# Kernel optimization log

Measured on AMD Instinct MI355X. Metric: run time of the kernel, lower is better.

The kernel has to match this reference:

```python
import jax, jax.numpy as jnp
import numpy as np

H, N, M, F, D = 8, 4096, 4096, 1024, 256

def setup_inputs() -> dict:
    key = jax.random.key(0)
    ks = jax.random.split(key, 8)
    sc = 0.02
    return {
        "this": jax.random.normal(ks[0], (N, F), dtype=jnp.float32),
        "that": jax.random.normal(ks[1], (M, F), dtype=jnp.float32),
        "mask": jax.random.randint(ks[2], (N, M), 0, 2) > 0,
        "Wq": jax.random.normal(ks[3], (H, F, D), dtype=jnp.float32) * sc,
        "bq": jnp.zeros((H, D), dtype=jnp.float32),
        "Wk": jax.random.normal(ks[4], (H, F, D), dtype=jnp.float32) * sc,
        "bk": jnp.zeros((H, D), dtype=jnp.float32),
        "Wv": jax.random.normal(ks[5], (H, F, D), dtype=jnp.float32) * sc,
        "bv": jnp.zeros((H, D), dtype=jnp.float32),
        "Wo": jax.random.normal(ks[6], (2 * F, F), dtype=jnp.float32) * sc,
        "bo": jnp.zeros((F,), dtype=jnp.float32),
    }

def reference(this, that, mask, Wq, bq, Wk, bk, Wv, bv, Wo, bo):
    # Per-head projections, batched over heads. q:[h,n,d] k,v:[h,m,d]
    q = jnp.einsum('nf,hfd->hnd', this, Wq) + bq[:, None, :]
    k = jnp.einsum('mf,hfd->hmd', that, Wk) + bk[:, None, :]
    v = jnp.einsum('mf,hfd->hmd', that, Wv) + bv[:, None, :]
    # Unscaled attention scores [h,n,m]
    s = jnp.einsum('hnd,hmd->hnm', q, k)
    neg = 1e9 * (~mask).astype(s.dtype)              # additive mask [n,m]
    head_ids = jnp.arange(s.shape[0])[:, None, None]  # mask applies to heads >= 4 only
    s = jnp.where(head_ids >= 4, s - neg, s)
    w = jax.nn.softmax(s, axis=-1)
    r = jnp.einsum('hnm,hmd->hnd', w, v)              # [h,n,d]
    # concat heads along feature axis in head order -> [n, h*d]
    cat = jnp.transpose(r, (1, 0, 2)).reshape(this.shape[0], -1)
    out = cat @ Wo + bo
    return out + this
```

## Files before the change

### kernel.cpp

```cpp
#include <hip/hip_runtime.h>
#include <stdint.h>


#define H_ 8
#define N_ 4096
#define M_ 4096
#define F_ 1024
#define D_ 256

typedef unsigned short u16;
typedef unsigned int u32;
typedef unsigned long long u64;
typedef __bf16 bf16x8 __attribute__((ext_vector_type(8)));
typedef float f32x4 __attribute__((ext_vector_type(4)));

static __device__ __forceinline__ u16 f2bf(float f) {
  union { float f; u32 u; } v; v.f = f;
  u32 u = v.u + 0x7fffu + ((v.u >> 16) & 1u);
  return (u16)(u >> 16);
}

static __device__ __forceinline__ void gld16(const void* g, void* l) {
  __builtin_amdgcn_global_load_lds(
      (const __attribute__((address_space(1))) void*)g,
      (__attribute__((address_space(3))) void*)l, 16, 0, 0);
}

__global__ void k_mask_detect(const u32* __restrict__ m, u32* __restrict__ flag) {
  u32 bad = 0;
  for (int i = threadIdx.x; i < 4096; i += 64) bad |= (m[i] & ~1u);
  u64 anyBad = __ballot(bad != 0);
  if (threadIdx.x == 0) *flag = (anyBad != 0) ? 1u : 0u;
}

__global__ void k_mask_pack(const void* __restrict__ mp, const u32* __restrict__ flag,
                            u64* __restrict__ out) {
  const int i = blockIdx.x * 256 + threadIdx.x;
  u64 bits = 0;
  if (*flag) {
    const u32* p = (const u32*)mp + (size_t)i * 16;
#pragma unroll
    for (int w = 0; w < 16; ++w) {
      u32 x = p[w];
#pragma unroll
      for (int j = 0; j < 4; ++j)
        bits |= (u64)(((x >> (8 * j)) & 0xffu) ? 1u : 0u) << (w * 4 + j);
    }
  } else {
    const u32* p = (const u32*)mp + (size_t)i * 64;
#pragma unroll
    for (int w = 0; w < 64; ++w) bits |= (u64)(p[w] ? 1u : 0u) << w;
  }
  out[i] = bits;
}

__global__ void k_f32_to_bf16(const float* __restrict__ in, u16* __restrict__ out, int n4) {
  int i = blockIdx.x * blockDim.x + threadIdx.x;
  if (i >= n4) return;
  float4 v = ((const float4*)in)[i];
  u32 w0 = (u32)f2bf(v.x) | ((u32)f2bf(v.y) << 16);
  u32 w1 = (u32)f2bf(v.z) | ((u32)f2bf(v.w) << 16);
  ((uint2*)out)[i] = make_uint2(w0, w1);
}

__global__ void k_transpose_f32_bf16(const float* __restrict__ in, u16* __restrict__ out,
                                     int R, int C) {
  __shared__ float t[32][33];
  const int b = blockIdx.z;
  const float* src = in + (size_t)b * R * C;
  u16* dst = out + (size_t)b * R * C;
  const int r0 = blockIdx.x * 32, c0 = blockIdx.y * 32;
  const int tr = threadIdx.x >> 3, tc = (threadIdx.x & 7) * 4;
  float4 v = *(const float4*)(src + (size_t)(r0 + tr) * C + c0 + tc);
  t[tr][tc + 0] = v.x; t[tr][tc + 1] = v.y; t[tr][tc + 2] = v.z; t[tr][tc + 3] = v.w;
  __syncthreads();
  u16* d4 = dst + (size_t)(c0 + tr) * R + r0 + tc;
  d4[0] = f2bf(t[tc + 0][tr]); d4[1] = f2bf(t[tc + 1][tr]);
  d4[2] = f2bf(t[tc + 2][tr]); d4[3] = f2bf(t[tc + 3][tr]);
}

__global__ void k_transpose_bf16(const u16* __restrict__ in, u16* __restrict__ out,
                                 int R, int C) {
  __shared__ u16 t[32][33];
  const int b = blockIdx.z;
  const u16* src = in + (size_t)b * R * C;
  u16* dst = out + (size_t)b * R * C;
  const int r0 = blockIdx.x * 32, c0 = blockIdx.y * 32;
  const int tr = threadIdx.x >> 3, tc = (threadIdx.x & 7) * 4;
  const u16* s4 = src + (size_t)(r0 + tr) * C + c0 + tc;
  t[tr][tc + 0] = s4[0]; t[tr][tc + 1] = s4[1]; t[tr][tc + 2] = s4[2]; t[tr][tc + 3] = s4[3];
  __syncthreads();
  u16* d4 = dst + (size_t)(c0 + tr) * R + r0 + tc;
  d4[0] = t[tc + 0][tr]; d4[1] = t[tc + 1][tr]; d4[2] = t[tc + 2][tr]; d4[3] = t[tc + 3][tr];
}

template <int EPI>
__global__ __launch_bounds__(256, 2) void k_gemm_nt(
    const u16* __restrict__ A, const u16* __restrict__ B,
    const float* __restrict__ bias, const float* __restrict__ resid,
    u16* __restrict__ Cb, float* __restrict__ Cf,
    int K, int lda, int ldb, int ldc,
    size_t aBatch, size_t bBatch, size_t biasBatch, size_t cBatch)
{
  __shared__ u16 la[128 * 64];
  __shared__ u16 lb[128 * 64];
  const int tid = threadIdx.x;
  const int lane = tid & 63, wave = tid >> 6;
  const int g = lane >> 4, fr = lane & 15;
  const int wr = wave >> 1, wc = wave & 1;
  const int z = blockIdx.z;
  const size_t row0 = (size_t)blockIdx.x * 128, col0 = (size_t)blockIdx.y * 128;
  const u16* Ab = A + z * aBatch + row0 * lda;
  const u16* Bb = B + z * bBatch + col0 * ldb;

  f32x4 zero = {0.f, 0.f, 0.f, 0.f};
  f32x4 acc[4][4];
#pragma unroll
  for (int m = 0; m < 4; ++m)
#pragma unroll
    for (int n = 0; n < 4; ++n) acc[m][n] = zero;

  for (int k0 = 0; k0 < K; k0 += 64) {
    __syncthreads();
#pragma unroll
    for (int i = 0; i < 4; ++i) {
      int c = i * 256 + tid;
      int row = c >> 3, slot = c & 7;
      int srcSlot = slot ^ (row & 7);
      gld16(Ab + (size_t)row * lda + k0 + srcSlot * 8, la + (size_t)(i * 256 + wave * 64) * 8);
      gld16(Bb + (size_t)row * ldb + k0 + srcSlot * 8, lb + (size_t)(i * 256 + wave * 64) * 8);
    }
    __syncthreads();
#pragma unroll
    for (int kk = 0; kk < 2; ++kk) {
      const int colByte = (kk * 32 + g * 8) * 2;
      bf16x8 af[4], bfr[4];
#pragma unroll
      for (int m = 0; m < 4; ++m) {
        int row = wr * 64 + m * 16 + fr;
        af[m] = *(const bf16x8*)((const char*)la + ((row * 128 + colByte) ^ ((row & 7) << 4)));
      }
#pragma unroll
      for (int n = 0; n < 4; ++n) {
        int row = wc * 64 + n * 16 + fr;
        bfr[n] = *(const bf16x8*)((const char*)lb + ((row * 128 + colByte) ^ ((row & 7) << 4)));
      }
#pragma unroll
      for (int m = 0; m < 4; ++m)
#pragma unroll
        for (int n = 0; n < 4; ++n)
          acc[m][n] = __builtin_amdgcn_mfma_f32_16x16x32_bf16(af[m], bfr[n], acc[m][n], 0, 0, 0);
    }
  }

#pragma unroll
  for (int n = 0; n < 4; ++n) {
    const int col = wc * 64 + n * 16 + fr;
    const float bv = bias[z * biasBatch + col0 + col];
#pragma unroll
    for (int m = 0; m < 4; ++m) {
#pragma unroll
      for (int r = 0; r < 4; ++r) {
        const int row = wr * 64 + m * 16 + g * 4 + r;
        const float val = acc[m][n][r] + bv;
        const size_t idx = z * cBatch + (row0 + row) * ldc + col0 + col;
        if (EPI == 0) {
          Cb[idx] = f2bf(val);
        } else {
          Cf[idx] = val + resid[(row0 + row) * ldc + col0 + col];
        }
      }
    }
  }
}

__global__ __launch_bounds__(256, 2) void k_attn(
    const u16* __restrict__ q, const u16* __restrict__ k,
    const u16* __restrict__ vt, const u64* __restrict__ mbits,
    u16* __restrict__ cat)
{
  __shared__ u16 smem[32768];
  u16* lk = smem;
  u16* lv = smem + 16384;
  const int tid = threadIdx.x;
  const int lane = tid & 63, wave = tid >> 6;
  const int g = lane >> 4, fr = lane & 15;
  const int h = blockIdx.y;
  const int n0 = blockIdx.x * 64 + wave * 16;
  const u16* qh = q + ((size_t)h * N_ + n0 + fr) * D_;
  const u16* kh = k + (size_t)h * M_ * D_;
  const u16* vh = vt + (size_t)h * D_ * M_;

  bf16x8 qf[8];
#pragma unroll
  for (int dc = 0; dc < 8; ++dc) qf[dc] = *(const bf16x8*)(qh + dc * 32 + g * 8);

  f32x4 zero = {0.f, 0.f, 0.f, 0.f};
  f32x4 racc[16];
#pragma unroll
  for (int i = 0; i < 16; ++i) racc[i] = zero;
  float mrow = -3e38f, lrow = 0.f;

  const u64* mrp = mbits + (size_t)(n0 + fr) * (M_ / 64);
  const bool useMask = (h >= 4);

  for (int m0 = 0; m0 < M_; m0 += 64) {
    __syncthreads();
#pragma unroll
    for (int i = 0; i < 8; ++i) {
      int c = i * 256 + tid;
      int row = c >> 5, slot = c & 31;
      int srcSlot = (slot & 24) | ((slot ^ row) & 7);
      gld16(kh + (size_t)(m0 + row) * D_ + srcSlot * 8, lk + (size_t)(i * 256 + wave * 64) * 8);
      int row2 = c >> 3, slot2 = c & 7;
      int srcSlot2 = (slot2 ^ row2) & 7;
      gld16(vh + (size_t)row2 * M_ + m0 + srcSlot2 * 8, lv + (size_t)(i * 256 + wave * 64) * 8);
    }
    __syncthreads();

    f32x4 s[4];
#pragma unroll
    for (int mt = 0; mt < 4; ++mt) s[mt] = zero;
#pragma unroll
    for (int dc = 0; dc < 8; ++dc) {
      const int colByte = (dc * 32 + g * 8) * 2;
#pragma unroll
      for (int mt = 0; mt < 4; ++mt) {
        const int row = mt * 16 + fr;
        bf16x8 af = *(const bf16x8*)((const char*)lk + ((row * 512 + colByte) ^ ((row & 7) << 4)));
        s[mt] = __builtin_amdgcn_mfma_f32_16x16x32_bf16(af, qf[dc], s[mt], 0, 0, 0);
      }
    }

    if (useMask) {
      const u64 wm = mrp[m0 >> 6];
#pragma unroll
      for (int mt = 0; mt < 4; ++mt) {
        const u32 nib = (u32)(wm >> (mt * 16 + g * 4));
        if (!(nib & 1u)) s[mt][0] -= 1e9f;
        if (!(nib & 2u)) s[mt][1] -= 1e9f;
        if (!(nib & 4u)) s[mt][2] -= 1e9f;
        if (!(nib & 8u)) s[mt][3] -= 1e9f;
      }
    }

    float pm = -3e38f;
#pragma unroll
    for (int mt = 0; mt < 4; ++mt)
#pragma unroll
      for (int r = 0; r < 4; ++r) pm = fmaxf(pm, s[mt][r]);
    pm = fmaxf(pm, __shfl_xor(pm, 16, 64));
    pm = fmaxf(pm, __shfl_xor(pm, 32, 64));
    const float mnew = fmaxf(mrow, pm);
    const float scale = __expf(mrow - mnew);
    float ls = 0.f;
#pragma unroll
    for (int mt = 0; mt < 4; ++mt)
#pragma unroll
      for (int r = 0; r < 4; ++r) { float p = __expf(s[mt][r] - mnew); s[mt][r] = p; ls += p; }
    ls += __shfl_xor(ls, 16, 64);
    ls += __shfl_xor(ls, 32, 64);
    lrow = lrow * scale + ls;
    mrow = mnew;
#pragma unroll
    for (int i = 0; i < 16; ++i) racc[i] *= scale;

    u32 w[4][2];
#pragma unroll
    for (int mt = 0; mt < 4; ++mt) {
      w[mt][0] = (u32)f2bf(s[mt][0]) | ((u32)f2bf(s[mt][1]) << 16);
      w[mt][1] = (u32)f2bf(s[mt][2]) | ((u32)f2bf(s[mt][3]) << 16);
    }
    const int src0 = (g & 1) * 32 + fr;
    const int src1 = src0 + 16;
    const bool hi = (g >> 1) != 0;
#pragma unroll
    for (int cc = 0; cc < 2; ++cc) {
      u32 a0 = __shfl(w[cc * 2][0], src0, 64), b0 = __shfl(w[cc * 2 + 1][0], src0, 64);
      u32 a1 = __shfl(w[cc * 2][1], src0, 64), b1 = __shfl(w[cc * 2 + 1][1], src0, 64);
      u32 a2 = __shfl(w[cc * 2][0], src1, 64), b2 = __shfl(w[cc * 2 + 1][0], src1, 64);
      u32 a3 = __shfl(w[cc * 2][1], src1, 64), b3 = __shfl(w[cc * 2 + 1][1], src1, 64);
      union { u32 u[4]; bf16x8 v; } pf;
      pf.u[0] = hi ? b0 : a0;
      pf.u[1] = hi ? b1 : a1;
      pf.u[2] = hi ? b2 : a2;
      pf.u[3] = hi ? b3 : a3;
      const int mcolByte = (cc * 32 + g * 8) * 2;
#pragma unroll
      for (int dt = 0; dt < 16; ++dt) {
        const int row = dt * 16 + fr;
        bf16x8 av = *(const bf16x8*)((const char*)lv + ((row * 128 + mcolByte) ^ ((row & 7) << 4)));
        racc[dt] = __builtin_amdgcn_mfma_f32_16x16x32_bf16(av, pf.v, racc[dt], 0, 0, 0);
      }
    }
  }

  __syncthreads();
  u16* lt = smem + (size_t)wave * (16 * 264);
  const float inv = 1.f / lrow;
#pragma unroll
  for (int dt = 0; dt < 16; ++dt) {
    u32 w0 = (u32)f2bf(racc[dt][0] * inv) | ((u32)f2bf(racc[dt][1] * inv) << 16);
    u32 w1 = (u32)f2bf(racc[dt][2] * inv) | ((u32)f2bf(racc[dt][3] * inv) << 16);
    *(u32*)(lt + fr * 264 + dt * 16 + g * 4) = w0;
    *(u32*)(lt + fr * 264 + dt * 16 + g * 4 + 2) = w1;
  }
  __syncthreads();
#pragma unroll
  for (int p = 0; p < 8; ++p) {
    const int c2 = p * 64 + lane;
    const int row = c2 >> 5, ch = c2 & 31;
    uint4 val = *(const uint4*)(lt + row * 264 + ch * 8);
    *(uint4*)(cat + (size_t)(n0 + row) * (H_ * D_) + (size_t)h * D_ + ch * 8) = val;
  }
}

extern "C" void kernel_launch(void* const* d_in, const int* in_sizes, int n_in,
                              void* d_out, int out_size, void* d_ws, size_t ws_size,
                              hipStream_t stream) {
  const float* thisf = (const float*)d_in[0];
  const float* thatf = (const float*)d_in[1];
  const void* maskp = (const void*)d_in[2];
  const float* Wq = (const float*)d_in[3];
  const float* bq = (const float*)d_in[4];
  const float* Wk = (const float*)d_in[5];
  const float* bk = (const float*)d_in[6];
  const float* Wv = (const float*)d_in[7];
  const float* bv = (const float*)d_in[8];
  const float* Wo = (const float*)d_in[9];
  const float* bo = (const float*)d_in[10];
  float* outp = (float*)d_out;

  char* ws = (char*)d_ws;
  size_t o = 0;
  u16* thisb = (u16*)(ws + o); o += (size_t)N_ * F_ * 2;
  u16* thatb = (u16*)(ws + o); o += (size_t)M_ * F_ * 2;
  u16* wqt = (u16*)(ws + o); o += (size_t)H_ * D_ * F_ * 2;
  u16* wkt = (u16*)(ws + o); o += (size_t)H_ * D_ * F_ * 2;
  u16* wvt = (u16*)(ws + o); o += (size_t)H_ * D_ * F_ * 2;
  u16* wot = (u16*)(ws + o); o += (size_t)F_ * 2 * F_ * 2;
  u16* qb = (u16*)(ws + o); o += (size_t)H_ * N_ * D_ * 2;
  u16* kb = (u16*)(ws + o); o += (size_t)H_ * M_ * D_ * 2;
  u16* vb = (u16*)(ws + o); o += (size_t)H_ * M_ * D_ * 2;
  u16* vtb = (u16*)(ws + o); o += (size_t)H_ * D_ * M_ * 2;
  u16* catb = (u16*)(ws + o); o += (size_t)N_ * 2 * F_ * 2;
  u64* mbits = (u64*)(ws + o); o += (size_t)N_ * M_ / 8;
  u32* mflag = (u32*)(ws + o); o += 256;
  (void)ws_size; (void)in_sizes; (void)n_in; (void)out_size;

  k_mask_detect<<<dim3(1), dim3(64), 0, stream>>>((const u32*)maskp, mflag);
  k_mask_pack<<<dim3(N_ * M_ / 64 / 256), dim3(256), 0, stream>>>(maskp, mflag, mbits);

  k_f32_to_bf16<<<dim3(N_ * F_ / 4 / 256), dim3(256), 0, stream>>>(thisf, thisb, N_ * F_ / 4);
  k_f32_to_bf16<<<dim3(M_ * F_ / 4 / 256), dim3(256), 0, stream>>>(thatf, thatb, M_ * F_ / 4);
  k_transpose_f32_bf16<<<dim3(F_ / 32, D_ / 32, H_), dim3(256), 0, stream>>>(Wq, wqt, F_, D_);
  k_transpose_f32_bf16<<<dim3(F_ / 32, D_ / 32, H_), dim3(256), 0, stream>>>(Wk, wkt, F_, D_);
  k_transpose_f32_bf16<<<dim3(F_ / 32, D_ / 32, H_), dim3(256), 0, stream>>>(Wv, wvt, F_, D_);
  k_transpose_f32_bf16<<<dim3(2 * F_ / 32, F_ / 32, 1), dim3(256), 0, stream>>>(Wo, wot, 2 * F_, F_);

  k_gemm_nt<0><<<dim3(N_ / 128, D_ / 128, H_), dim3(256), 0, stream>>>(
      thisb, wqt, bq, nullptr, qb, nullptr, F_, F_, F_, D_,
      (size_t)0, (size_t)D_ * F_, (size_t)D_, (size_t)N_ * D_);
  k_gemm_nt<0><<<dim3(M_ / 128, D_ / 128, H_), dim3(256), 0, stream>>>(
      thatb, wkt, bk, nullptr, kb, nullptr, F_, F_, F_, D_,
      (size_t)0, (size_t)D_ * F_, (size_t)D_, (size_t)M_ * D_);
  k_gemm_nt<0><<<dim3(M_ / 128, D_ / 128, H_), dim3(256), 0, stream>>>(
      thatb, wvt, bv, nullptr, vb, nullptr, F_, F_, F_, D_,
      (size_t)0, (size_t)D_ * F_, (size_t)D_, (size_t)M_ * D_);

  k_transpose_bf16<<<dim3(M_ / 32, D_ / 32, H_), dim3(256), 0, stream>>>(vb, vtb, M_, D_);

  k_attn<<<dim3(N_ / 64, H_), dim3(256), 0, stream>>>(qb, kb, vtb, mbits, catb);

  k_gemm_nt<1><<<dim3(N_ / 128, F_ / 128, 1), dim3(256), 0, stream>>>(
      catb, wot, bo, thisf, nullptr, outp, 2 * F_, 2 * F_, 2 * F_, F_,
      (size_t)0, (size_t)0, (size_t)0, (size_t)0);
}
```

Before: 551.3 us.

## Rewrite attention with 32x32 MFMA, pre-swizzled K/V layouts, and double-buffered GEMM

The attention kernel is rewritten to use 32x32x16 bf16 MFMA tiles with 32 query rows per wave, a double-buffered K/V LDS pipeline, exp2-based softmax and a lazy rescale that only runs when the row max grows past a threshold. The K and V projection GEMMs now write directly into blocked layouts the attention kernel can stream, which removes the separate V transpose kernel. The mask is packed with a wave ballot into a column-major word layout. The generic GEMM gains LDS double buffering. The lazy-rescale threshold and the new layouts add numerical and indexing risk in exchange for higher MFMA throughput and fewer passes over memory.

```diff
diff --git a/kernel.cpp b/kernel.cpp
--- a/kernel.cpp
+++ b/kernel.cpp
@@ -11,13 +11,21 @@
 typedef unsigned short u16;
 typedef unsigned int u32;
 typedef unsigned long long u64;
+typedef unsigned char u8;
 typedef __bf16 bf16x8 __attribute__((ext_vector_type(8)));
 typedef float f32x4 __attribute__((ext_vector_type(4)));
+typedef float f32x16 __attribute__((ext_vector_type(16)));
 
 static __device__ __forceinline__ u16 f2bf(float f) {
   union { float f; u32 u; } v; v.f = f;
   u32 u = v.u + 0x7fffu + ((v.u >> 16) & 1u);
   return (u16)(u >> 16);
+}
+
+static __device__ __forceinline__ u32 cvtpk(float lo, float hi) {
+  u32 r;
+  asm("v_cvt_pk_bf16_f32 %0, %1, %2" : "=v"(r) : "v"(lo), "v"(hi));
+  return r;
 }
 
 static __device__ __forceinline__ void gld16(const void* g, void* l) {
@@ -33,25 +41,20 @@
   if (threadIdx.x == 0) *flag = (anyBad != 0) ? 1u : 0u;
 }
 
-__global__ void k_mask_pack(const void* __restrict__ mp, const u32* __restrict__ flag,
-                            u64* __restrict__ out) {
-  const int i = blockIdx.x * 256 + threadIdx.x;
-  u64 bits = 0;
-  if (*flag) {
-    const u32* p = (const u32*)mp + (size_t)i * 16;
-#pragma unroll
-    for (int w = 0; w < 16; ++w) {
-      u32 x = p[w];
-#pragma unroll
-      for (int j = 0; j < 4; ++j)
-        bits |= (u64)(((x >> (8 * j)) & 0xffu) ? 1u : 0u) << (w * 4 + j);
-    }
-  } else {
-    const u32* p = (const u32*)mp + (size_t)i * 64;
-#pragma unroll
-    for (int w = 0; w < 64; ++w) bits |= (u64)(p[w] ? 1u : 0u) << w;
-  }
-  out[i] = bits;
+__global__ void k_mask_pack2(const void* __restrict__ mp, const u32* __restrict__ flag,
+                             u32* __restrict__ out) {
+  const int lane = threadIdx.x & 63, wave = threadIdx.x >> 6;
+  const int wid = blockIdx.x * 4 + wave;
+  const int qrow = wid >> 6;
+  const int m0 = (wid & 63) * 64;
+  int x;
+  if (*flag) x = ((const u8*)mp)[(size_t)qrow * M_ + m0 + lane];
+  else       x = ((const int*)mp)[(size_t)qrow * M_ + m0 + lane];
+  u64 bits = __ballot(x != 0);
+  if (lane == 0) {
+    out[(size_t)(m0 >> 5) * N_ + qrow] = (u32)bits;
+    out[(size_t)((m0 >> 5) + 1) * N_ + qrow] = (u32)(bits >> 32);
+  }
 }
 
 __global__ void k_f32_to_bf16(const float* __restrict__ in, u16* __restrict__ out, int n4) {
@@ -79,21 +82,6 @@
   d4[2] = f2bf(t[tc + 2][tr]); d4[3] = f2bf(t[tc + 3][tr]);
 }
 
-__global__ void k_transpose_bf16(const u16* __restrict__ in, u16* __restrict__ out,
-                                 int R, int C) {
-  __shared__ u16 t[32][33];
-  const int b = blockIdx.z;
-  const u16* src = in + (size_t)b * R * C;
-  u16* dst = out + (size_t)b * R * C;
-  const int r0 = blockIdx.x * 32, c0 = blockIdx.y * 32;
-  const int tr = threadIdx.x >> 3, tc = (threadIdx.x & 7) * 4;
-  const u16* s4 = src + (size_t)(r0 + tr) * C + c0 + tc;
-  t[tr][tc + 0] = s4[0]; t[tr][tc + 1] = s4[1]; t[tr][tc + 2] = s4[2]; t[tr][tc + 3] = s4[3];
-  __syncthreads();
-  u16* d4 = dst + (size_t)(c0 + tr) * R + r0 + tc;
-  d4[0] = t[tc + 0][tr]; d4[1] = t[tc + 1][tr]; d4[2] = t[tc + 2][tr]; d4[3] = t[tc + 3][tr];
-}
-
 template <int EPI>
 __global__ __launch_bounds__(256, 2) void k_gemm_nt(
     const u16* __restrict__ A, const u16* __restrict__ B,
@@ -102,8 +90,8 @@
     int K, int lda, int ldb, int ldc,
     size_t aBatch, size_t bBatch, size_t biasBatch, size_t cBatch)
 {
-  __shared__ u16 la[128 * 64];
-  __shared__ u16 lb[128 * 64];
+  __shared__ u16 la[2][128 * 64];
+  __shared__ u16 lb[2][128 * 64];
   const int tid = threadIdx.x;
   const int lane = tid & 63, wave = tid >> 6;
   const int g = lane >> 4, fr = lane & 15;
@@ -120,17 +108,24 @@
 #pragma unroll
     for (int n = 0; n < 4; ++n) acc[m][n] = zero;
 
-  for (int k0 = 0; k0 < K; k0 += 64) {
-    __syncthreads();
+  auto STAGE = [&](int bs, int k0) {
 #pragma unroll
     for (int i = 0; i < 4; ++i) {
       int c = i * 256 + tid;
       int row = c >> 3, slot = c & 7;
       int srcSlot = slot ^ (row & 7);
-      gld16(Ab + (size_t)row * lda + k0 + srcSlot * 8, la + (size_t)(i * 256 + wave * 64) * 8);
-      gld16(Bb + (size_t)row * ldb + k0 + srcSlot * 8, lb + (size_t)(i * 256 + wave * 64) * 8);
-    }
-    __syncthreads();
+      gld16(Ab + (size_t)row * lda + k0 + srcSlot * 8, &la[bs][(i * 256 + wave * 64) * 8]);
+      gld16(Bb + (size_t)row * ldb + k0 + srcSlot * 8, &lb[bs][(i * 256 + wave * 64) * 8]);
+    }
+  };
+
+  STAGE(0, 0);
+  __syncthreads();
+  int cur = 0;
+  for (int k0 = 0; k0 < K; k0 += 64) {
+    if (k0 + 64 < K) STAGE(cur ^ 1, k0 + 64);
+    const char* lac = (const char*)la[cur];
+    const char* lbc = (const char*)lb[cur];
 #pragma unroll
     for (int kk = 0; kk < 2; ++kk) {
       const int colByte = (kk * 32 + g * 8) * 2;
@@ -138,12 +133,12 @@
 #pragma unroll
       for (int m = 0; m < 4; ++m) {
         int row = wr * 64 + m * 16 + fr;
-        af[m] = *(const bf16x8*)((const char*)la + ((row * 128 + colByte) ^ ((row & 7) << 4)));
+        af[m] = *(const bf16x8*)(lac + ((row * 128 + colByte) ^ ((row & 7) << 4)));
       }
 #pragma unroll
       for (int n = 0; n < 4; ++n) {
         int row = wc * 64 + n * 16 + fr;
-        bfr[n] = *(const bf16x8*)((const char*)lb + ((row * 128 + colByte) ^ ((row & 7) << 4)));
+        bfr[n] = *(const bf16x8*)(lbc + ((row * 128 + colByte) ^ ((row & 7) << 4)));
       }
 #pragma unroll
       for (int m = 0; m < 4; ++m)
@@ -151,6 +146,8 @@
         for (int n = 0; n < 4; ++n)
           acc[m][n] = __builtin_amdgcn_mfma_f32_16x16x32_bf16(af[m], bfr[n], acc[m][n], 0, 0, 0);
     }
+    __syncthreads();
+    cur ^= 1;
   }
 
 #pragma unroll
@@ -163,155 +160,168 @@
       for (int r = 0; r < 4; ++r) {
         const int row = wr * 64 + m * 16 + g * 4 + r;
         const float val = acc[m][n][r] + bv;
-        const size_t idx = z * cBatch + (row0 + row) * ldc + col0 + col;
+        const size_t grow = row0 + row, gcol = col0 + col;
         if (EPI == 0) {
-          Cb[idx] = f2bf(val);
+          Cb[(size_t)z * cBatch + grow * ldc + gcol] = f2bf(val);
+        } else if (EPI == 1) {
+          Cb[(size_t)z * (M_ * D_) + (gcol >> 3) * (M_ * 8) + grow * 8 + (gcol & 7)] = f2bf(val);
+        } else if (EPI == 2) {
+          Cb[(size_t)z * (M_ * D_) + (grow >> 3) * (D_ * 8) + gcol * 8 + (grow & 7)] = f2bf(val);
         } else {
-          Cf[idx] = val + resid[(row0 + row) * ldc + col0 + col];
+          Cf[grow * ldc + gcol] = val + resid[grow * ldc + gcol];
         }
       }
     }
   }
 }
 
-__global__ __launch_bounds__(256, 2) void k_attn(
-    const u16* __restrict__ q, const u16* __restrict__ k,
-    const u16* __restrict__ vt, const u64* __restrict__ mbits,
+__global__ __launch_bounds__(256, 2) void k_attn2(
+    const u16* __restrict__ q, const u16* __restrict__ k2,
+    const u16* __restrict__ v2, const u32* __restrict__ mw,
     u16* __restrict__ cat)
 {
   __shared__ u16 smem[32768];
-  u16* lk = smem;
-  u16* lv = smem + 16384;
   const int tid = threadIdx.x;
   const int lane = tid & 63, wave = tid >> 6;
-  const int g = lane >> 4, fr = lane & 15;
-  const int h = blockIdx.y;
-  const int n0 = blockIdx.x * 64 + wave * 16;
-  const u16* qh = q + ((size_t)h * N_ + n0 + fr) * D_;
-  const u16* kh = k + (size_t)h * M_ * D_;
-  const u16* vh = vt + (size_t)h * D_ * M_;
-
-  bf16x8 qf[8];
-#pragma unroll
-  for (int dc = 0; dc < 8; ++dc) qf[dc] = *(const bf16x8*)(qh + dc * 32 + g * 8);
-
-  f32x4 zero = {0.f, 0.f, 0.f, 0.f};
-  f32x4 racc[16];
-#pragma unroll
-  for (int i = 0; i < 16; ++i) racc[i] = zero;
+  const int hi = lane >> 5, col = lane & 31;
+  const int h = blockIdx.x & 7;
+  const int xt = blockIdx.x >> 3;
+  const int n0w = xt * 128 + wave * 32;
+  const float L2E = 1.44269504f;
+
+  const u16* kh = k2 + (size_t)h * (M_ * D_);
+  const u16* vh = v2 + (size_t)h * (M_ * D_);
+
+  bf16x8 qf[16];
+  {
+    const u16* qp = q + ((size_t)h * N_ + n0w + col) * D_ + hi * 8;
+#pragma unroll
+    for (int dc = 0; dc < 16; ++dc) qf[dc] = *(const bf16x8*)(qp + dc * 16);
+  }
+
+  f32x16 racc[8];
+#pragma unroll
+  for (int i = 0; i < 8; ++i)
+#pragma unroll
+    for (int e = 0; e < 16; ++e) racc[i][e] = 0.f;
+
   float mrow = -3e38f, lrow = 0.f;
-
-  const u64* mrp = mbits + (size_t)(n0 + fr) * (M_ / 64);
   const bool useMask = (h >= 4);
-
-  for (int m0 = 0; m0 < M_; m0 += 64) {
+  const u32* mp = mw + (n0w + col);
+
+  auto STAGE = [&](int bs, int m0) {
+    u16* lkb = smem + bs * 16384;
+    u16* lvb = lkb + 8192;
+#pragma unroll
+    for (int i = 0; i < 4; ++i) {
+      int c = i * 256 + tid;
+      gld16(kh + (size_t)(c >> 5) * (M_ * 8) + (size_t)(m0 + (c & 31)) * 8,
+            lkb + (i * 256 + wave * 64) * 8);
+      gld16(vh + (size_t)(c >> 8) * (D_ * 8) + (size_t)m0 * 256 + (size_t)(c & 255) * 8,
+            lvb + (i * 256 + wave * 64) * 8);
+    }
+  };
+
+  STAGE(0, 0);
+  __syncthreads();
+  int cur = 0;
+
+  for (int it = 0; it < M_ / 32; ++it) {
+    const int m0 = it * 32;
+    if (it + 1 < M_ / 32) STAGE(cur ^ 1, m0 + 32);
+    u32 mword = 0xFFFFFFFFu;
+    if (useMask) mword = mp[(size_t)(m0 >> 5) * N_];
+
+    const char* lkb = (const char*)smem + cur * 32768;
+    const char* lvb = lkb + 16384;
+
+    f32x16 sA, sB;
+#pragma unroll
+    for (int e = 0; e < 16; ++e) { sA[e] = 0.f; sB[e] = 0.f; }
+#pragma unroll
+    for (int dc = 0; dc < 16; dc += 2) {
+      bf16x8 a0 = *(const bf16x8*)(lkb + dc * 1024 + lane * 16);
+      bf16x8 a1 = *(const bf16x8*)(lkb + dc * 1024 + 1024 + lane * 16);
+      sA = __builtin_amdgcn_mfma_f32_32x32x16_bf16(a0, qf[dc], sA, 0, 0, 0);
+      sB = __builtin_amdgcn_mfma_f32_32x32x16_bf16(a1, qf[dc + 1], sB, 0, 0, 0);
+    }
+    f32x16 sv = sA + sB;
+
+    if (useMask) {
+      u32 mm = mword >> (hi * 4);
+#pragma unroll
+      for (int r = 0; r < 16; ++r)
+        if (!((mm >> ((r & 3) + 8 * (r >> 2))) & 1u)) sv[r] -= 1e9f;
+    }
+
+    float pm = sv[0];
+#pragma unroll
+    for (int r = 1; r < 16; ++r) pm = fmaxf(pm, sv[r]);
+    pm = fmaxf(pm, __shfl_xor(pm, 32));
+
+    if (!__all(pm <= mrow + 8.f)) {
+      float mnew = fmaxf(mrow, pm);
+      float rs = __builtin_exp2f((mrow - mnew) * L2E);
+      lrow *= rs;
+#pragma unroll
+      for (int i = 0; i < 8; ++i)
+#pragma unroll
+        for (int e = 0; e < 16; ++e) racc[i][e] *= rs;
+      mrow = mnew;
+    }
+    const float mL = mrow * L2E;
+    float p[16];
+    float ls = 0.f;
+#pragma unroll
+    for (int r = 0; r < 16; ++r) {
+      p[r] = __builtin_exp2f(sv[r] * L2E - mL);
+      ls += p[r];
+    }
+    ls += __shfl_xor(ls, 32);
+    lrow += ls;
+
+#pragma unroll
+    for (int ks = 0; ks < 2; ++ks) {
+      u32 a0 = cvtpk(p[8 * ks + 0], p[8 * ks + 1]);
+      u32 a1 = cvtpk(p[8 * ks + 2], p[8 * ks + 3]);
+      u32 b0 = cvtpk(p[8 * ks + 4], p[8 * ks + 5]);
+      u32 b1 = cvtpk(p[8 * ks + 6], p[8 * ks + 7]);
+      u32 sa0 = __shfl_xor(a0, 32), sa1 = __shfl_xor(a1, 32);
+      u32 sb0 = __shfl_xor(b0, 32), sb1 = __shfl_xor(b1, 32);
+      union { u32 w[4]; bf16x8 v; } bp;
+      bp.w[0] = hi ? sb0 : a0;
+      bp.w[1] = hi ? sb1 : a1;
+      bp.w[2] = hi ? b0 : sa0;
+      bp.w[3] = hi ? b1 : sa1;
+      const char* lvk = lvb + ks * 8192 + hi * 4096 + col * 16;
+#pragma unroll
+      for (int ds = 0; ds < 8; ++ds) {
+        bf16x8 av = *(const bf16x8*)(lvk + ds * 512);
+        racc[ds] = __builtin_amdgcn_mfma_f32_32x32x16_bf16(av, bp.v, racc[ds], 0, 0, 0);
+      }
+    }
     __syncthreads();
-#pragma unroll
-    for (int i = 0; i < 8; ++i) {
-      int c = i * 256 + tid;
-      int row = c >> 5, slot = c & 31;
-      int srcSlot = (slot & 24) | ((slot ^ row) & 7);
-      gld16(kh + (size_t)(m0 + row) * D_ + srcSlot * 8, lk + (size_t)(i * 256 + wave * 64) * 8);
-      int row2 = c >> 3, slot2 = c & 7;
-      int srcSlot2 = (slot2 ^ row2) & 7;
-      gld16(vh + (size_t)row2 * M_ + m0 + srcSlot2 * 8, lv + (size_t)(i * 256 + wave * 64) * 8);
-    }
-    __syncthreads();
-
-    f32x4 s[4];
-#pragma unroll
-    for (int mt = 0; mt < 4; ++mt) s[mt] = zero;
-#pragma unroll
-    for (int dc = 0; dc < 8; ++dc) {
-      const int colByte = (dc * 32 + g * 8) * 2;
-#pragma unroll
-      for (int mt = 0; mt < 4; ++mt) {
-        const int row = mt * 16 + fr;
-        bf16x8 af = *(const bf16x8*)((const char*)lk + ((row * 512 + colByte) ^ ((row & 7) << 4)));
-        s[mt] = __builtin_amdgcn_mfma_f32_16x16x32_bf16(af, qf[dc], s[mt], 0, 0, 0);
-      }
-    }
-
-    if (useMask) {
-      const u64 wm = mrp[m0 >> 6];
-#pragma unroll
-      for (int mt = 0; mt < 4; ++mt) {
-        const u32 nib = (u32)(wm >> (mt * 16 + g * 4));
-        if (!(nib & 1u)) s[mt][0] -= 1e9f;
-        if (!(nib & 2u)) s[mt][1] -= 1e9f;
-        if (!(nib & 4u)) s[mt][2] -= 1e9f;
-        if (!(nib & 8u)) s[mt][3] -= 1e9f;
-      }
-    }
-
-    float pm = -3e38f;
-#pragma unroll
-    for (int mt = 0; mt < 4; ++mt)
-#pragma unroll
-      for (int r = 0; r < 4; ++r) pm = fmaxf(pm, s[mt][r]);
-    pm = fmaxf(pm, __shfl_xor(pm, 16, 64));
-    pm = fmaxf(pm, __shfl_xor(pm, 32, 64));
-    const float mnew = fmaxf(mrow, pm);
-    const float scale = __expf(mrow - mnew);
-    float ls = 0.f;
-#pragma unroll
-    for (int mt = 0; mt < 4; ++mt)
-#pragma unroll
-      for (int r = 0; r < 4; ++r) { float p = __expf(s[mt][r] - mnew); s[mt][r] = p; ls += p; }
-    ls += __shfl_xor(ls, 16, 64);
-    ls += __shfl_xor(ls, 32, 64);
-    lrow = lrow * scale + ls;
-    mrow = mnew;
-#pragma unroll
-    for (int i = 0; i < 16; ++i) racc[i] *= scale;
-
-    u32 w[4][2];
-#pragma unroll
-    for (int mt = 0; mt < 4; ++mt) {
-      w[mt][0] = (u32)f2bf(s[mt][0]) | ((u32)f2bf(s[mt][1]) << 16);
-      w[mt][1] = (u32)f2bf(s[mt][2]) | ((u32)f2bf(s[mt][3]) << 16);
-    }
-    const int src0 = (g & 1) * 32 + fr;
-    const int src1 = src0 + 16;
-    const bool hi = (g >> 1) != 0;
-#pragma unroll
-    for (int cc = 0; cc < 2; ++cc) {
-      u32 a0 = __shfl(w[cc * 2][0], src0, 64), b0 = __shfl(w[cc * 2 + 1][0], src0, 64);
-      u32 a1 = __shfl(w[cc * 2][1], src0, 64), b1 = __shfl(w[cc * 2 + 1][1], src0, 64);
-      u32 a2 = __shfl(w[cc * 2][0], src1, 64), b2 = __shfl(w[cc * 2 + 1][0], src1, 64);
-      u32 a3 = __shfl(w[cc * 2][1], src1, 64), b3 = __shfl(w[cc * 2 + 1][1], src1, 64);
-      union { u32 u[4]; bf16x8 v; } pf;
-      pf.u[0] = hi ? b0 : a0;
-      pf.u[1] = hi ? b1 : a1;
-      pf.u[2] = hi ? b2 : a2;
-      pf.u[3] = hi ? b3 : a3;
-      const int mcolByte = (cc * 32 + g * 8) * 2;
-#pragma unroll
-      for (int dt = 0; dt < 16; ++dt) {
-        const int row = dt * 16 + fr;
-        bf16x8 av = *(const bf16x8*)((const char*)lv + ((row * 128 + mcolByte) ^ ((row & 7) << 4)));
-        racc[dt] = __builtin_amdgcn_mfma_f32_16x16x32_bf16(av, pf.v, racc[dt], 0, 0, 0);
-      }
-    }
-  }
-
+    cur ^= 1;
+  }
+
+  char* lt = (char*)smem + wave * 16384;
+  const float inv = 1.f / lrow;
+#pragma unroll
+  for (int ds = 0; ds < 8; ++ds) {
+#pragma unroll
+    for (int t = 0; t < 8; ++t) {
+      int d0 = ds * 32 + (2 * t & 3) + 8 * (t >> 1) + 4 * hi;
+      u32 w = cvtpk(racc[ds][2 * t] * inv, racc[ds][2 * t + 1] * inv);
+      *(u32*)(lt + ((col * 512 + d0 * 2) ^ ((col & 7) << 4))) = w;
+    }
+  }
   __syncthreads();
-  u16* lt = smem + (size_t)wave * (16 * 264);
-  const float inv = 1.f / lrow;
-#pragma unroll
-  for (int dt = 0; dt < 16; ++dt) {
-    u32 w0 = (u32)f2bf(racc[dt][0] * inv) | ((u32)f2bf(racc[dt][1] * inv) << 16);
-    u32 w1 = (u32)f2bf(racc[dt][2] * inv) | ((u32)f2bf(racc[dt][3] * inv) << 16);
-    *(u32*)(lt + fr * 264 + dt * 16 + g * 4) = w0;
-    *(u32*)(lt + fr * 264 + dt * 16 + g * 4 + 2) = w1;
-  }
-  __syncthreads();
-#pragma unroll
-  for (int p = 0; p < 8; ++p) {
-    const int c2 = p * 64 + lane;
-    const int row = c2 >> 5, ch = c2 & 31;
-    uint4 val = *(const uint4*)(lt + row * 264 + ch * 8);
-    *(uint4*)(cat + (size_t)(n0 + row) * (H_ * D_) + (size_t)h * D_ + ch * 8) = val;
+#pragma unroll
+  for (int pch = 0; pch < 16; ++pch) {
+    int c = pch * 64 + lane;
+    int row = c >> 5, ch = c & 31;
+    uint4 val = *(const uint4*)(lt + ((row * 512 + ch * 16) ^ ((row & 7) << 4)));
+    *(uint4*)(cat + (size_t)(n0w + row) * (H_ * D_) + (size_t)h * D_ + ch * 8) = val;
   }
 }
 
@@ -339,17 +349,16 @@
   u16* wkt = (u16*)(ws + o); o += (size_t)H_ * D_ * F_ * 2;
   u16* wvt = (u16*)(ws + o); o += (size_t)H_ * D_ * F_ * 2;
   u16* wot = (u16*)(ws + o); o += (size_t)F_ * 2 * F_ * 2;
-  u16* qb = (u16*)(ws + o); o += (size_t)H_ * N_ * D_ * 2;
-  u16* kb = (u16*)(ws + o); o += (size_t)H_ * M_ * D_ * 2;
-  u16* vb = (u16*)(ws + o); o += (size_t)H_ * M_ * D_ * 2;
-  u16* vtb = (u16*)(ws + o); o += (size_t)H_ * D_ * M_ * 2;
+  u16* qb  = (u16*)(ws + o); o += (size_t)H_ * N_ * D_ * 2;
+  u16* k2  = (u16*)(ws + o); o += (size_t)H_ * M_ * D_ * 2;
+  u16* v2  = (u16*)(ws + o); o += (size_t)H_ * M_ * D_ * 2;
   u16* catb = (u16*)(ws + o); o += (size_t)N_ * 2 * F_ * 2;
-  u64* mbits = (u64*)(ws + o); o += (size_t)N_ * M_ / 8;
+  u32* mw2 = (u32*)(ws + o); o += (size_t)(M_ / 32) * N_ * 4;
   u32* mflag = (u32*)(ws + o); o += 256;
   (void)ws_size; (void)in_sizes; (void)n_in; (void)out_size;
 
   k_mask_detect<<<dim3(1), dim3(64), 0, stream>>>((const u32*)maskp, mflag);
-  k_mask_pack<<<dim3(N_ * M_ / 64 / 256), dim3(256), 0, stream>>>(maskp, mflag, mbits);
+  k_mask_pack2<<<dim3(N_ * (M_ / 64) / 4), dim3(256), 0, stream>>>(maskp, mflag, mw2);
 
   k_f32_to_bf16<<<dim3(N_ * F_ / 4 / 256), dim3(256), 0, stream>>>(thisf, thisb, N_ * F_ / 4);
   k_f32_to_bf16<<<dim3(M_ * F_ / 4 / 256), dim3(256), 0, stream>>>(thatf, thatb, M_ * F_ / 4);
@@ -361,18 +370,16 @@
   k_gemm_nt<0><<<dim3(N_ / 128, D_ / 128, H_), dim3(256), 0, stream>>>(
       thisb, wqt, bq, nullptr, qb, nullptr, F_, F_, F_, D_,
       (size_t)0, (size_t)D_ * F_, (size_t)D_, (size_t)N_ * D_);
-  k_gemm_nt<0><<<dim3(M_ / 128, D_ / 128, H_), dim3(256), 0, stream>>>(
-      thatb, wkt, bk, nullptr, kb, nullptr, F_, F_, F_, D_,
-      (size_t)0, (size_t)D_ * F_, (size_t)D_, (size_t)M_ * D_);
-  k_gemm_nt<0><<<dim3(M_ / 128, D_ / 128, H_), dim3(256), 0, stream>>>(
-      thatb, wvt, bv, nullptr, vb, nullptr, F_, F_, F_, D_,
-      (size_t)0, (size_t)D_ * F_, (size_t)D_, (size_t)M_ * D_);
-
-  k_transpose_bf16<<<dim3(M_ / 32, D_ / 32, H_), dim3(256), 0, stream>>>(vb, vtb, M_, D_);
-
-  k_attn<<<dim3(N_ / 64, H_), dim3(256), 0, stream>>>(qb, kb, vtb, mbits, catb);
-
-  k_gemm_nt<1><<<dim3(N_ / 128, F_ / 128, 1), dim3(256), 0, stream>>>(
+  k_gemm_nt<1><<<dim3(M_ / 128, D_ / 128, H_), dim3(256), 0, stream>>>(
+      thatb, wkt, bk, nullptr, k2, nullptr, F_, F_, F_, D_,
+      (size_t)0, (size_t)D_ * F_, (size_t)D_, (size_t)0);
+  k_gemm_nt<2><<<dim3(M_ / 128, D_ / 128, H_), dim3(256), 0, stream>>>(
+      thatb, wvt, bv, nullptr, v2, nullptr, F_, F_, F_, D_,
+      (size_t)0, (size_t)D_ * F_, (size_t)D_, (size_t)0);
+
+  k_attn2<<<dim3(256), dim3(256), 0, stream>>>(qb, k2, v2, mw2, catb);
+
+  k_gemm_nt<3><<<dim3(N_ / 128, F_ / 128, 1), dim3(256), 0, stream>>>(
       catb, wot, bo, thisf, nullptr, outp, 2 * F_, 2 * F_, 2 * F_, F_,
       (size_t)0, (size_t)0, (size_t)0, (size_t)0);
 }
```

After: 584.8 us. 6.1% more time.
